# Kernel tuning notes

Hardware: AMD Instinct MI355X
Metric: run time of the kernel (lower is better)

Reference implementation:

```python
import jax, jax.numpy as jnp
import numpy as np

LN_EPS = 1e-5
NORM_EPS = 1e-12
TEMPERATURE = 0.5


def _project(h, W1, b1, W2, b2, g, beta):
    # projection head: Linear -> ReLU -> Linear -> LayerNorm, then L2 normalize
    x = jnp.maximum(h @ W1 + b1, 0.0) @ W2 + b2          # [B, P]
    mu = jnp.mean(x, axis=-1, keepdims=True)
    var = jnp.mean(jnp.square(x - mu), axis=-1, keepdims=True)
    x = (x - mu) * jax.lax.rsqrt(var + LN_EPS) * g + beta
    n = jnp.linalg.norm(x, axis=-1, keepdims=True)
    return x / jnp.maximum(n, NORM_EPS)                   # [B, P]


def setup_inputs() -> dict:
    key = jax.random.key(0)
    ks = jax.random.split(key, 8)
    B, H, P, K, NBUF = 16384, 2048, 256, 64, 2000
    Hh = H // 2
    return {
        "hidden_states": jax.random.normal(ks[0], (B, H), jnp.float32),
        "positive_hidden": jax.random.normal(ks[1], (B, H), jnp.float32),
        "neg_buffer": jax.random.normal(ks[2], (NBUF, P), jnp.float32),
        "W1": jax.random.normal(ks[3], (H, Hh), jnp.float32) * (1.0 / np.sqrt(H)),
        "b1": jnp.zeros((Hh,), jnp.float32),
        "W2": jax.random.normal(ks[4], (Hh, P), jnp.float32) * (1.0 / np.sqrt(Hh)),
        "b2": jnp.zeros((P,), jnp.float32),
        "ln_gamma": jnp.ones((P,), jnp.float32),
        "ln_beta": jnp.zeros((P,), jnp.float32),
        "neg_indices": jax.random.randint(ks[5], (B, K), 0, NBUF, jnp.int32),
    }


def reference(hidden_states, positive_hidden, neg_buffer, W1, b1, W2, b2,
              ln_gamma, ln_beta, neg_indices):
    anchors = _project(hidden_states, W1, b1, W2, b2, ln_gamma, ln_beta)      # [B,P]
    positives = _project(positive_hidden, W1, b1, W2, b2, ln_gamma, ln_beta)  # [B,P]
    # negatives are detached in the original (buffer stores .detach() features)
    negs = jax.lax.stop_gradient(neg_buffer)[neg_indices]                      # [B,K,P]
    pos_sim = jnp.einsum('bp,bp->b', anchors, positives) / TEMPERATURE        # [B]
    neg_sims = jnp.einsum('bkp,bp->bk', negs, anchors) / TEMPERATURE          # [B,K]
    logits = jnp.concatenate([pos_sim[:, None], neg_sims], axis=1)            # [B,1+K]
    # cross-entropy with label 0 for every anchor, averaged over the batch
    loss = -jnp.mean(jax.nn.log_softmax(logits, axis=-1)[:, 0])
    return loss
```

## Files before the change

### kernel.cpp

```cpp
#include <hip/hip_runtime.h>
#include <hip/hip_bf16.h>
#include <cstdint>

#define BATCH   16384
#define HDIM    2048
#define HHDIM   1024
#define PDIM    256
#define KNEG    64
#define NBUF    2000
#define M1      (2 * BATCH)

typedef float  f32x4  __attribute__((ext_vector_type(4)));
typedef __bf16 bf16x8 __attribute__((ext_vector_type(8)));

typedef __attribute__((address_space(3))) unsigned int       lds_u32;
typedef __attribute__((address_space(1))) const unsigned int glb_u32;

__device__ __forceinline__ void gload_lds16(const void* g, void* l) {
  __builtin_amdgcn_global_load_lds((glb_u32*)g, (lds_u32*)l, 16, 0, 0);
}

#define VMCNT(n) asm volatile("s_waitcnt vmcnt(" #n ")" ::: "memory")
#define LGKM(n)  asm volatile("s_waitcnt lgkmcnt(" #n ")" ::: "memory")

__global__ __launch_bounds__(256)
void cast_bf16_kernel(const float* __restrict__ src, __bf16* __restrict__ dst,
                      long n8) {
  long i = (long)blockIdx.x * blockDim.x + threadIdx.x;
  long stride = (long)gridDim.x * blockDim.x;
  for (; i < n8; i += stride) {
    f32x4 a = ((const f32x4*)src)[2 * i];
    f32x4 b = ((const f32x4*)src)[2 * i + 1];
    bf16x8 w;
    for (int j = 0; j < 4; ++j) { w[j] = (__bf16)a[j]; w[4 + j] = (__bf16)b[j]; }
    ((bf16x8*)dst)[i] = w;
  }
}

__global__ void transpose_cast_kernel(const float* __restrict__ src,
                                      __bf16* __restrict__ dst, int K, int N) {
  __shared__ float tile[32][33];
  int bn = blockIdx.x * 32, bk = blockIdx.y * 32;
  int tx = threadIdx.x, ty = threadIdx.y;
  for (int j = 0; j < 32; j += 8)
    tile[ty + j][tx] = src[(size_t)(bk + ty + j) * N + bn + tx];
  __syncthreads();
  for (int j = 0; j < 32; j += 8)
    dst[(size_t)(bn + ty + j) * K + bk + tx] = (__bf16)tile[tx][ty + j];
}

template <int KD, int NBt, int GRID>
__global__ __launch_bounds__(512)
void gemm_f32a(const float* __restrict__ A0, const float* __restrict__ A1v,
               const __bf16* __restrict__ Bt, const float* __restrict__ bias,
               __bf16* __restrict__ C) {
  constexpr int KT   = KD / 32;
  constexpr int NDIM = NBt * 256;

  __shared__ float  lAf[2 * 2 * 4096];
  __shared__ __bf16 lBf[2 * 2 * 4096];

  constexpr int Q = GRID / 8;
  int bid = blockIdx.x;
  int swb = (bid & 7) * Q + (bid >> 3);
  const int mb = swb / NBt, nb = swb % NBt;
  const long mrow0 = (long)mb * 256;
  const int  ncol0 = nb * 256;

  const float* Af = (mrow0 < BATCH) ? (A0 + mrow0 * (long)KD)
                                    : (A1v + (mrow0 - BATCH) * (long)KD);

  const int tid = threadIdx.x;
  const int wid = tid >> 6, lane = tid & 63;
  const int wr = wid >> 2, wc = wid & 3;
  const int fl = lane & 15, fh = lane >> 4;

  int aoffs[4][2];
  #pragma unroll
  for (int mi = 0; mi < 4; ++mi)
    #pragma unroll
    for (int p = 0; p < 2; ++p) {
      int row = wr * 64 + mi * 16 + fl;
      aoffs[mi][p] = row * 32 + (((2 * fh + p) ^ (row & 7)) * 4);
    }
  int boffs[2];
  #pragma unroll
  for (int ni = 0; ni < 2; ++ni) {
    int row = wc * 32 + ni * 16 + fl;
    boffs[ni] = row * 32 + ((fh ^ ((row >> 1) & 3)) * 8);
  }

  const int r0a = tid >> 3, ssa = (tid & 7) ^ ((tid >> 3) & 7);
  const int r0b = tid >> 2, ssb = (tid & 3) ^ (((tid >> 2) >> 1) & 3);
  const int dwA = wid * 256;
  const int dwB = wid * 512;

  auto stA = [&](int h, int t) {
    float* base = lAf + (t & 1) * 8192 + h * 4096 + dwA;
    const float* s0 = Af + (size_t)(h * 128 + r0a) * KD + t * 32 + ssa * 4;
    gload_lds16(s0, (void*)base);
    gload_lds16(s0 + (size_t)64 * KD, (void*)(base + 2048));
  };
  auto stB = [&](int h, int t) {
    __bf16* base = lBf + (t & 1) * 8192 + h * 4096 + dwB;
    gload_lds16(Bt + (size_t)(ncol0 + h * 128 + r0b) * KD + t * 32 + ssb * 8,
                (void*)base);
  };

  f32x4  aA[4][2];
  bf16x8 areg[4], breg0[2], breg1[2];

  auto loadAraw = [&](int mh, int s) {
    const float* base = lAf + (s & 1) * 8192 + mh * 4096;
    #pragma unroll
    for (int mi = 0; mi < 4; ++mi)
      #pragma unroll
      for (int p = 0; p < 2; ++p)
        aA[mi][p] = *(const f32x4*)(base + aoffs[mi][p]);
  };
  auto cvtA = [&]() {
    #pragma unroll
    for (int mi = 0; mi < 4; ++mi)
      #pragma unroll
      for (int j = 0; j < 4; ++j) {
        areg[mi][j]     = (__bf16)aA[mi][0][j];
        areg[mi][4 + j] = (__bf16)aA[mi][1][j];
      }
  };
  auto loadB = [&](bf16x8 (&br)[2], int nh, int s) {
    const __bf16* base = lBf + (s & 1) * 8192 + nh * 4096;
    #pragma unroll
    for (int ni = 0; ni < 2; ++ni)
      br[ni] = *(const bf16x8*)(base + boffs[ni]);
  };

  f32x4 acc[2][2][4][2] = {};

#define QMFMA(mh, nh, BR)                                                     \
  __builtin_amdgcn_s_setprio(1);                                              \
  _Pragma("unroll")                                                           \
  for (int mi = 0; mi < 4; ++mi) {                                            \
    _Pragma("unroll")                                                         \
    for (int ni = 0; ni < 2; ++ni)                                            \
      acc[mh][nh][mi][ni] = __builtin_amdgcn_mfma_f32_16x16x32_bf16(          \
          areg[mi], BR[ni], acc[mh][nh][mi][ni], 0, 0, 0);                    \
  }                                                                           \
  __builtin_amdgcn_s_setprio(0);

  stA(0, 0); stB(0, 0); stA(1, 0); stB(1, 0);
  stA(0, 1); stB(1, 1); stB(0, 1); stA(1, 1);
  VMCNT(6);
  __builtin_amdgcn_s_barrier();
  __builtin_amdgcn_sched_barrier(0);

  for (int s = 0; s < KT; ++s) {
    loadAraw(0, s);
    loadB(breg0, 0, s);
    if (s >= 1 && s + 1 < KT) stB(0, s + 1);
    __builtin_amdgcn_s_barrier();
    LGKM(0);
    __builtin_amdgcn_sched_barrier(0);
    cvtA();
    QMFMA(0, 0, breg0);
    __builtin_amdgcn_s_barrier();

    loadB(breg1, 1, s);
    if (s >= 1 && s + 1 < KT) stA(1, s + 1);
    __builtin_amdgcn_s_barrier();
    LGKM(0);
    __builtin_amdgcn_sched_barrier(0);
    QMFMA(0, 1, breg1);
    __builtin_amdgcn_s_barrier();

    loadAraw(1, s);
    if (s + 2 < KT) stA(0, s + 2);
    __builtin_amdgcn_s_barrier();
    LGKM(0);
    __builtin_amdgcn_sched_barrier(0);
    cvtA();
    QMFMA(1, 1, breg1);
    __builtin_amdgcn_s_barrier();

    if (s + 2 < KT) stB(1, s + 2);
    __builtin_amdgcn_s_barrier();
    __builtin_amdgcn_sched_barrier(0);
    QMFMA(1, 0, breg0);
    if (s + 2 < KT) { VMCNT(3); } else { VMCNT(0); }
    __builtin_amdgcn_s_barrier();
    __builtin_amdgcn_sched_barrier(0);
  }

#undef QMFMA

  #pragma unroll
  for (int mh = 0; mh < 2; ++mh)
    #pragma unroll
    for (int nh = 0; nh < 2; ++nh)
      #pragma unroll
      for (int ni = 0; ni < 2; ++ni) {
        int col = ncol0 + nh * 128 + wc * 32 + ni * 16 + fl;
        float bv = bias[col];
        #pragma unroll
        for (int mi = 0; mi < 4; ++mi)
          #pragma unroll
          for (int r = 0; r < 4; ++r) {
            long row = mrow0 + mh * 128 + wr * 64 + mi * 16 + fh * 4 + r;
            float v = fmaxf(acc[mh][nh][mi][ni][r] + bv, 0.0f);
            C[row * NDIM + col] = (__bf16)v;
          }
      }
}

template <int KD, int BMH, int NBt, bool RELU_OUT, bool LNFUSE, int GRID>
__global__ __launch_bounds__(512)
void gemm_8ph(const __bf16* __restrict__ A, const __bf16* __restrict__ Bt,
              const float* __restrict__ bias,
              const float* __restrict__ lng, const float* __restrict__ lnb,
              void* __restrict__ Cv) {
  static_assert(!LNFUSE || NBt == 1, "LN fusion needs full rows per block");
  constexpr int KT    = KD / 64;
  constexpr int MI    = BMH / 32;
  constexpr int AHALF = BMH * 64;
  constexpr int BHALF = 128 * 64;
  constexpr int ASTEP = 2 * AHALF;
  constexpr int BSTEP = 2 * BHALF;
  constexpr int NDIM  = NBt * 256;
  constexpr int AUL   = BMH / 64;

  __shared__ __bf16 lA[2 * ASTEP];
  __shared__ __bf16 lB[2 * BSTEP];

  constexpr int Q = GRID / 8;
  int bid = blockIdx.x;
  int swb = (bid & 7) * Q + (bid >> 3);
  const int mb = swb / NBt, nb = swb % NBt;
  const long mrow0 = (long)mb * (2 * BMH);
  const int  ncol0 = nb * 256;

  const int tid = threadIdx.x;
  const int wid = tid >> 6, lane = tid & 63;
  const int wr = wid >> 2, wc = wid & 3;
  const int fl = lane & 15, fh = lane >> 4;

  int aoff[MI][2], boff[2][2];
  #pragma unroll
  for (int mi = 0; mi < MI; ++mi)
    #pragma unroll
    for (int ks = 0; ks < 2; ++ks) {
      int row = wr * (BMH / 2) + mi * 16 + fl;
      aoff[mi][ks] = row * 64 + (((ks * 4 + fh) ^ (row & 7)) * 8);
    }
  #pragma unroll
  for (int ni = 0; ni < 2; ++ni)
    #pragma unroll
    for (int ks = 0; ks < 2; ++ks) {
      int row = wc * 32 + ni * 16 + fl;
      boff[ni][ks] = row * 64 + (((ks * 4 + fh) ^ (row & 7)) * 8);
    }

  const int r0 = tid >> 3, sl = tid & 7;
  long aS[2][AUL], bS[2][2];
  #pragma unroll
  for (int h = 0; h < 2; ++h) {
    #pragma unroll
    for (int i = 0; i < AUL; ++i) {
      int rr = r0 + i * 64;
      int ss = sl ^ (rr & 7);
      aS[h][i] = (mrow0 + h * BMH + rr) * (long)KD + ss * 8;
    }
    #pragma unroll
    for (int i = 0; i < 2; ++i) {
      int rr = r0 + i * 64;
      int ss = sl ^ (rr & 7);
      bS[h][i] = ((long)(ncol0 + h * 128 + rr)) * KD + ss * 8;
    }
  }
  const int dstw = wid * 512;

  auto stA = [&](int h, int t) {
    __bf16* base = lA + (t & 1) * ASTEP + h * AHALF + dstw;
    #pragma unroll
    for (int i = 0; i < AUL; ++i)
      gload_lds16(A + aS[h][i] + (long)t * 64, (void*)(base + i * 4096));
  };
  auto stB = [&](int h, int t) {
    __bf16* base = lB + (t & 1) * BSTEP + h * BHALF + dstw;
    #pragma unroll
    for (int i = 0; i < 2; ++i)
      gload_lds16(Bt + bS[h][i] + (long)t * 64, (void*)(base + i * 4096));
  };

  bf16x8 aregA[MI][2], aregB[MI][2], breg0[2][2], breg1[2][2];
  auto loadA = [&](bf16x8 (&ar)[MI][2], int mh, int s) {
    const __bf16* base = lA + (s & 1) * ASTEP + mh * AHALF;
    #pragma unroll
    for (int mi = 0; mi < MI; ++mi)
      #pragma unroll
      for (int ks = 0; ks < 2; ++ks)
        ar[mi][ks] = *(const bf16x8*)(base + aoff[mi][ks]);
  };
  auto loadB = [&](bf16x8 (&br)[2][2], int nh, int s) {
    const __bf16* base = lB + (s & 1) * BSTEP + nh * BHALF;
    #pragma unroll
    for (int ni = 0; ni < 2; ++ni)
      #pragma unroll
      for (int ks = 0; ks < 2; ++ks)
        br[ni][ks] = *(const bf16x8*)(base + boff[ni][ks]);
  };

  f32x4 acc[2][2][MI][2] = {};

#define PHASE_MFMA(mh, nh, AR, BR)                                            \
  __builtin_amdgcn_s_setprio(1);                                              \
  _Pragma("unroll")                                                           \
  for (int ks = 0; ks < 2; ++ks) {                                            \
    _Pragma("unroll")                                                         \
    for (int mi = 0; mi < MI; ++mi) {                                         \
      _Pragma("unroll")                                                       \
      for (int ni = 0; ni < 2; ++ni)                                          \
        acc[mh][nh][mi][ni] = __builtin_amdgcn_mfma_f32_16x16x32_bf16(        \
            AR[mi][ks], BR[ni][ks], acc[mh][nh][mi][ni], 0, 0, 0);            \
    }                                                                         \
  }                                                                           \
  __builtin_amdgcn_s_setprio(0);

  stA(0, 0); stB(0, 0); stA(1, 0); stB(1, 0);
  stA(0, 1); stB(1, 1); stB(0, 1); stA(1, 1);
  if constexpr (AUL == 2) { VMCNT(8); } else { VMCNT(6); }
  __builtin_amdgcn_s_barrier();
  __builtin_amdgcn_sched_barrier(0);
  loadA(aregA, 0, 0);
  loadB(breg0, 0, 0);

  for (int s = 0; s < KT; ++s) {
    if (s >= 1 && s + 1 < KT) stB(0, s + 1);
    loadB(breg1, 1, s);
    PHASE_MFMA(0, 0, aregA, breg0);
    if (s + 1 < KT) {
      if constexpr (AUL == 2) { VMCNT(6); } else { VMCNT(5); }
    } else {
      VMCNT(0);
    }
    __builtin_amdgcn_s_barrier();
    __builtin_amdgcn_sched_barrier(0);

    if (s >= 1 && s + 1 < KT) stA(1, s + 1);
    loadA(aregB, 1, s);
    PHASE_MFMA(0, 1, aregA, breg1);
    __builtin_amdgcn_s_barrier();
    __builtin_amdgcn_sched_barrier(0);

    if (s + 2 < KT) stA(0, s + 2);
    PHASE_MFMA(1, 1, aregB, breg1);
    if (s + 2 < KT) {
      if constexpr (AUL == 2) { VMCNT(4); } else { VMCNT(2); }
    } else if (s + 1 < KT) {
      if constexpr (AUL == 2) { VMCNT(2); } else { VMCNT(1); }
    } else {
      VMCNT(0);
    }
    __builtin_amdgcn_s_barrier();
    __builtin_amdgcn_sched_barrier(0);

    if (s + 2 < KT) stB(1, s + 2);
    PHASE_MFMA(1, 0, aregB, breg0);
    if (s + 1 < KT) {
      loadA(aregA, 0, s + 1);
      loadB(breg0, 0, s + 1);
    }
    __builtin_amdgcn_s_barrier();
    __builtin_amdgcn_sched_barrier(0);
  }

#undef PHASE_MFMA

  if constexpr (LNFUSE) {
    float (*s1p)[4] = (float(*)[4])((float*)lA);
    float (*s2p)[4] = (float(*)[4])((float*)lA + 512);
    float (*n2p)[4] = (float(*)[4])((float*)lA + 1024);

    float v[2][2][MI][2][4];
    float gg[2][2], bb[2][2];
    #pragma unroll
    for (int nh = 0; nh < 2; ++nh)
      #pragma unroll
      for (int ni = 0; ni < 2; ++ni) {
        int c = nh * 128 + wc * 32 + ni * 16 + fl;
        float bv = bias[c];
        gg[nh][ni] = lng[c]; bb[nh][ni] = lnb[c];
        #pragma unroll
        for (int mh = 0; mh < 2; ++mh)
          #pragma unroll
          for (int mi = 0; mi < MI; ++mi)
            #pragma unroll
            for (int r = 0; r < 4; ++r)
              v[mh][nh][mi][ni][r] = acc[mh][nh][mi][ni][r] + bv;
      }

    #pragma unroll
    for (int mh = 0; mh < 2; ++mh)
      #pragma unroll
      for (int mi = 0; mi < MI; ++mi)
        #pragma unroll
        for (int r = 0; r < 4; ++r) {
          float s1 = 0.0f, s2 = 0.0f;
          #pragma unroll
          for (int nh = 0; nh < 2; ++nh)
            #pragma unroll
            for (int ni = 0; ni < 2; ++ni) {
              float x = v[mh][nh][mi][ni][r];
              s1 += x; s2 += x * x;
            }
          for (int m = 1; m < 16; m <<= 1) {
            s1 += __shfl_xor(s1, m, 64);
            s2 += __shfl_xor(s2, m, 64);
          }
          if (fl == 0) {
            int lr = mh * 64 + wr * 32 + mi * 16 + fh * 4 + r;
            s1p[lr][wc] = s1; s2p[lr][wc] = s2;
          }
        }
    __syncthreads();

    float n2loc[2][MI][4];
    #pragma unroll
    for (int mh = 0; mh < 2; ++mh)
      #pragma unroll
      for (int mi = 0; mi < MI; ++mi)
        #pragma unroll
        for (int r = 0; r < 4; ++r) {
          int lr = mh * 64 + wr * 32 + mi * 16 + fh * 4 + r;
          float t1 = s1p[lr][0] + s1p[lr][1] + s1p[lr][2] + s1p[lr][3];
          float t2 = s2p[lr][0] + s2p[lr][1] + s2p[lr][2] + s2p[lr][3];
          float mu = t1 * (1.0f / PDIM);
          float var = t2 * (1.0f / PDIM) - mu * mu;
          float rstd = rsqrtf(var + 1e-5f);
          float n2 = 0.0f;
          #pragma unroll
          for (int nh = 0; nh < 2; ++nh)
            #pragma unroll
            for (int ni = 0; ni < 2; ++ni) {
              float y = (v[mh][nh][mi][ni][r] - mu) * rstd * gg[nh][ni] + bb[nh][ni];
              v[mh][nh][mi][ni][r] = y;
              n2 += y * y;
            }
          for (int m = 1; m < 16; m <<= 1) n2 += __shfl_xor(n2, m, 64);
          n2loc[mh][mi][r] = n2;
        }
    #pragma unroll
    for (int mh = 0; mh < 2; ++mh)
      #pragma unroll
      for (int mi = 0; mi < MI; ++mi)
        #pragma unroll
        for (int r = 0; r < 4; ++r)
          if (fl == 0) {
            int lr = mh * 64 + wr * 32 + mi * 16 + fh * 4 + r;
            n2p[lr][wc] = n2loc[mh][mi][r];
          }
    __syncthreads();

    #pragma unroll
    for (int mh = 0; mh < 2; ++mh)
      #pragma unroll
      for (int mi = 0; mi < MI; ++mi)
        #pragma unroll
        for (int r = 0; r < 4; ++r) {
          int lr = mh * 64 + wr * 32 + mi * 16 + fh * 4 + r;
          float t = n2p[lr][0] + n2p[lr][1] + n2p[lr][2] + n2p[lr][3];
          float sc = 1.0f / fmaxf(sqrtf(t), 1e-12f);
          #pragma unroll
          for (int nh = 0; nh < 2; ++nh)
            #pragma unroll
            for (int ni = 0; ni < 2; ++ni) {
              int c = nh * 128 + wc * 32 + ni * 16 + fl;
              ((float*)Cv)[(mrow0 + lr) * NDIM + c] = v[mh][nh][mi][ni][r] * sc;
            }
        }
  } else {
    #pragma unroll
    for (int mh = 0; mh < 2; ++mh)
      #pragma unroll
      for (int nh = 0; nh < 2; ++nh)
        #pragma unroll
        for (int ni = 0; ni < 2; ++ni) {
          int col = ncol0 + nh * 128 + wc * 32 + ni * 16 + fl;
          float bv = bias[col];
          #pragma unroll
          for (int mi = 0; mi < MI; ++mi)
            #pragma unroll
            for (int r = 0; r < 4; ++r) {
              long row = mrow0 + mh * BMH + wr * (BMH / 2) + mi * 16 + fh * 4 + r;
              float x = acc[mh][nh][mi][ni][r] + bv;
              if constexpr (RELU_OUT) {
                x = fmaxf(x, 0.0f);
                ((__bf16*)Cv)[row * NDIM + col] = (__bf16)x;
              } else {
                ((float*)Cv)[row * NDIM + col] = x;
              }
            }
        }
  }
}

__global__ __launch_bounds__(256)
void loss_kernel(const float* __restrict__ X, const __bf16* __restrict__ negb,
                 const int* __restrict__ nidx, float* __restrict__ partials) {
  __shared__ float lsum[4];
  int b    = blockIdx.x * 4 + (threadIdx.x >> 6);
  int lane = threadIdx.x & 63;
  int g = lane >> 4, lg = lane & 15;

  const float* arow = X + (size_t)b * PDIM;
  const float* prow = X + (size_t)(BATCH + b) * PDIM;

  float a16[16];
  #pragma unroll
  for (int j = 0; j < 4; ++j) {
    f32x4 av = *(const f32x4*)(arow + lg * 16 + j * 4);
    #pragma unroll
    for (int e = 0; e < 4; ++e) a16[j * 4 + e] = av[e];
  }

  float ps = 0.0f;
  #pragma unroll
  for (int j = 0; j < 4; ++j) {
    f32x4 p = *(const f32x4*)(prow + lg * 16 + j * 4);
    #pragma unroll
    for (int e = 0; e < 4; ++e) ps += a16[j * 4 + e] * p[e];
  }
  for (int m = 1; m < 16; m <<= 1) ps += __shfl_xor(ps, m, 64);
  float pos = ps * 2.0f;

  float myneg = -3.0e38f;
  for (int k4 = 0; k4 < 16; ++k4) {
    int k = k4 * 4 + g;
    int idx = nidx[(size_t)b * KNEG + k];
    const __bf16* nrow = negb + (size_t)idx * PDIM;
    float sv = 0.0f;
    #pragma unroll
    for (int j = 0; j < 2; ++j) {
      bf16x8 nv = *(const bf16x8*)(nrow + lg * 16 + j * 8);
      #pragma unroll
      for (int e = 0; e < 8; ++e) sv += a16[j * 8 + e] * (float)nv[e];
    }
    for (int m = 1; m < 16; m <<= 1) sv += __shfl_xor(sv, m, 64);
    if (lg == k4) myneg = sv * 2.0f;
  }

  float mx = myneg;
  for (int m = 1; m < 64; m <<= 1) mx = fmaxf(mx, __shfl_xor(mx, m, 64));
  mx = fmaxf(mx, pos);
  float e = expf(myneg - mx);
  for (int m = 1; m < 64; m <<= 1) e += __shfl_xor(e, m, 64);
  float tot = e + expf(pos - mx);
  float lb = -(pos - mx - logf(tot));

  if (lane == 0) lsum[threadIdx.x >> 6] = lb;
  __syncthreads();
  if (threadIdx.x == 0)
    partials[blockIdx.x] = lsum[0] + lsum[1] + lsum[2] + lsum[3];
}

__global__ void finalize_kernel(const float* __restrict__ partials,
                                float* __restrict__ out) {
  __shared__ float ls[4];
  int tid = threadIdx.x;
  float s = 0.0f;
  for (int i = tid; i < 4096; i += 256) s += partials[i];
  for (int m = 1; m < 64; m <<= 1) s += __shfl_xor(s, m, 64);
  if ((tid & 63) == 0) ls[tid >> 6] = s;
  __syncthreads();
  if (tid == 0) out[0] = (ls[0] + ls[1] + ls[2] + ls[3]) * (1.0f / BATCH);
}

extern "C" void kernel_launch(void* const* d_in, const int* in_sizes, int n_in,
                              void* d_out, int out_size, void* d_ws, size_t ws_size,
                              hipStream_t stream) {
  const float* hidden   = (const float*)d_in[0];
  const float* positive = (const float*)d_in[1];
  const float* negbuf   = (const float*)d_in[2];
  const float* W1       = (const float*)d_in[3];
  const float* b1       = (const float*)d_in[4];
  const float* W2       = (const float*)d_in[5];
  const float* b2       = (const float*)d_in[6];
  const float* gamma    = (const float*)d_in[7];
  const float* beta     = (const float*)d_in[8];
  const int*   nidx     = (const int*)d_in[9];
  float* out = (float*)d_out;

  char* ws = (char*)d_ws;
  const size_t OFF_W1T  = 67108864;
  const size_t OFF_W2T  = OFF_W1T + 4194304;
  const size_t OFF_NEGB = OFF_W2T + 524288;
  const size_t OFF_PART = OFF_NEGB + 1048576;
  const size_t OFF_X    = OFF_PART + 16384;

  __bf16* Y1       = (__bf16*)(ws);
  __bf16* W1T      = (__bf16*)(ws + OFF_W1T);
  __bf16* W2T      = (__bf16*)(ws + OFF_W2T);
  __bf16* negb     = (__bf16*)(ws + OFF_NEGB);
  float*  partials = (float*) (ws + OFF_PART);
  float*  X        = (float*) (ws + OFF_X);

  transpose_cast_kernel<<<dim3(HHDIM / 32, HDIM / 32), dim3(32, 8), 0, stream>>>(
      W1, W1T, HDIM, HHDIM);
  transpose_cast_kernel<<<dim3(PDIM / 32, HHDIM / 32), dim3(32, 8), 0, stream>>>(
      W2, W2T, HHDIM, PDIM);
  cast_bf16_kernel<<<256, 256, 0, stream>>>(negbuf, negb, (long)NBUF * PDIM / 8);

  gemm_f32a<HDIM, HHDIM / 256, (M1 / 256) * (HHDIM / 256)>
      <<<(M1 / 256) * (HHDIM / 256), 512, 0, stream>>>(
          hidden, positive, W1T, b1, Y1);

  gemm_8ph<HHDIM, 64, PDIM / 256, false, true, (M1 / 128) * (PDIM / 256)>
      <<<(M1 / 128) * (PDIM / 256), 512, 0, stream>>>(
          Y1, W2T, b2, gamma, beta, X);

  loss_kernel<<<BATCH / 4, 256, 0, stream>>>(X, negb, nidx, partials);
  finalize_kernel<<<1, 256, 0, stream>>>(partials, out);
}
```

Measured before the change: 308.1 us.

## Load GEMM A operand directly from global into registers, bypassing LDS

Removes the LDS staging buffer for the fp32 A operand. Each wave now issues its own global vector loads for its A fragments into two register sets (aA0/aA1), double-buffered across half-steps, while B still goes through LDS via global_load_lds. The goal is to cut LDS traffic, LDS footprint and a barrier stage. The cost is that the four column-waves each re-read the same A rows from global/L2, register pressure rises, and the vmcnt bookkeeping must be retuned.

```diff
diff --git a/kernel.cpp b/kernel.cpp
--- a/kernel.cpp
+++ b/kernel.cpp
@@ -57,7 +57,6 @@
   constexpr int KT   = KD / 32;
   constexpr int NDIM = NBt * 256;
 
-  __shared__ float  lAf[2 * 2 * 4096];
   __shared__ __bf16 lBf[2 * 2 * 4096];
 
   constexpr int Q = GRID / 8;
@@ -75,14 +74,14 @@
   const int wr = wid >> 2, wc = wid & 3;
   const int fl = lane & 15, fh = lane >> 4;
 
-  int aoffs[4][2];
-  #pragma unroll
-  for (int mi = 0; mi < 4; ++mi)
-    #pragma unroll
-    for (int p = 0; p < 2; ++p) {
-      int row = wr * 64 + mi * 16 + fl;
-      aoffs[mi][p] = row * 32 + (((2 * fh + p) ^ (row & 7)) * 4);
-    }
+  const float* aPtr[2][4];
+  #pragma unroll
+  for (int mh = 0; mh < 2; ++mh)
+    #pragma unroll
+    for (int mi = 0; mi < 4; ++mi)
+      aPtr[mh][mi] = Af + (size_t)(mh * 128 + wr * 64 + mi * 16 + fl) * KD
+                        + fh * 8;
+
   int boffs[2];
   #pragma unroll
   for (int ni = 0; ni < 2; ++ni) {
@@ -90,41 +89,32 @@
     boffs[ni] = row * 32 + ((fh ^ ((row >> 1) & 3)) * 8);
   }
 
-  const int r0a = tid >> 3, ssa = (tid & 7) ^ ((tid >> 3) & 7);
   const int r0b = tid >> 2, ssb = (tid & 3) ^ (((tid >> 2) >> 1) & 3);
-  const int dwA = wid * 256;
   const int dwB = wid * 512;
 
-  auto stA = [&](int h, int t) {
-    float* base = lAf + (t & 1) * 8192 + h * 4096 + dwA;
-    const float* s0 = Af + (size_t)(h * 128 + r0a) * KD + t * 32 + ssa * 4;
-    gload_lds16(s0, (void*)base);
-    gload_lds16(s0 + (size_t)64 * KD, (void*)(base + 2048));
-  };
   auto stB = [&](int h, int t) {
     __bf16* base = lBf + (t & 1) * 8192 + h * 4096 + dwB;
     gload_lds16(Bt + (size_t)(ncol0 + h * 128 + r0b) * KD + t * 32 + ssb * 8,
                 (void*)base);
   };
 
-  f32x4  aA[4][2];
+  f32x4  aA0[4][2], aA1[4][2];
   bf16x8 areg[4], breg0[2], breg1[2];
 
-  auto loadAraw = [&](int mh, int s) {
-    const float* base = lAf + (s & 1) * 8192 + mh * 4096;
+  auto issueA = [&](f32x4 (&dst)[4][2], int mh, int t) {
     #pragma unroll
     for (int mi = 0; mi < 4; ++mi)
       #pragma unroll
       for (int p = 0; p < 2; ++p)
-        aA[mi][p] = *(const f32x4*)(base + aoffs[mi][p]);
-  };
-  auto cvtA = [&]() {
+        dst[mi][p] = *(const f32x4*)(aPtr[mh][mi] + t * 32 + p * 4);
+  };
+  auto cvtA = [&](f32x4 (&src)[4][2]) {
     #pragma unroll
     for (int mi = 0; mi < 4; ++mi)
       #pragma unroll
       for (int j = 0; j < 4; ++j) {
-        areg[mi][j]     = (__bf16)aA[mi][0][j];
-        areg[mi][4 + j] = (__bf16)aA[mi][1][j];
+        areg[mi][j]     = (__bf16)src[mi][0][j];
+        areg[mi][4 + j] = (__bf16)src[mi][1][j];
       }
   };
   auto loadB = [&](bf16x8 (&br)[2], int nh, int s) {
@@ -147,45 +137,40 @@
   }                                                                           \
   __builtin_amdgcn_s_setprio(0);
 
-  stA(0, 0); stB(0, 0); stA(1, 0); stB(1, 0);
-  stA(0, 1); stB(1, 1); stB(0, 1); stA(1, 1);
-  VMCNT(6);
+  stB(0, 0); stB(1, 0); stB(0, 1); stB(1, 1);
+  issueA(aA0, 0, 0);
+  VMCNT(10);
   __builtin_amdgcn_s_barrier();
   __builtin_amdgcn_sched_barrier(0);
 
   for (int s = 0; s < KT; ++s) {
-    loadAraw(0, s);
     loadB(breg0, 0, s);
     if (s >= 1 && s + 1 < KT) stB(0, s + 1);
+    issueA(aA1, 1, s);
     __builtin_amdgcn_s_barrier();
     LGKM(0);
     __builtin_amdgcn_sched_barrier(0);
-    cvtA();
+    cvtA(aA0);
     QMFMA(0, 0, breg0);
     __builtin_amdgcn_s_barrier();
 
     loadB(breg1, 1, s);
-    if (s >= 1 && s + 1 < KT) stA(1, s + 1);
     __builtin_amdgcn_s_barrier();
     LGKM(0);
     __builtin_amdgcn_sched_barrier(0);
     QMFMA(0, 1, breg1);
     __builtin_amdgcn_s_barrier();
 
-    loadAraw(1, s);
-    if (s + 2 < KT) stA(0, s + 2);
-    __builtin_amdgcn_s_barrier();
-    LGKM(0);
-    __builtin_amdgcn_sched_barrier(0);
-    cvtA();
+    if (s + 2 < KT) stB(1, s + 2);
+    if (s + 1 < KT) issueA(aA0, 0, s + 1);
+    cvtA(aA1);
     QMFMA(1, 1, breg1);
     __builtin_amdgcn_s_barrier();
 
-    if (s + 2 < KT) stB(1, s + 2);
-    __builtin_amdgcn_s_barrier();
-    __builtin_amdgcn_sched_barrier(0);
     QMFMA(1, 0, breg0);
-    if (s + 2 < KT) { VMCNT(3); } else { VMCNT(0); }
+    if (s + 2 < KT)      { VMCNT(9); }
+    else if (s + 1 < KT) { VMCNT(8); }
+    else                 { VMCNT(0); }
     __builtin_amdgcn_s_barrier();
     __builtin_amdgcn_sched_barrier(0);
   }
```

After: 667.7 us. +116.7%, slower.
